# Optimization experiments

Hardware: AMD Instinct MI355X
Metric: run time of the kernel (lower is better)

The kernel has to match this reference:

```python
import jax, jax.numpy as jnp
import numpy as np

H1, W1GRID, K_SIZE, B = 28, 28, 5, 512
K2 = K_SIZE * K_SIZE  # 25 kernel weight matrices
_BITS = np.array([[0, 0], [0, 1], [1, 0], [1, 1]])  # 2^dim basis combos


def _grid_edges(h, w):
    """8-neighborhood grid graph; returns (src, dst, pseudo in [0,1]^2)."""
    ys, xs = np.meshgrid(np.arange(h), np.arange(w), indexing='ij')
    node = (ys * w + xs).reshape(-1)
    ys, xs = ys.reshape(-1), xs.reshape(-1)
    srcs, dsts, pses = [], [], []
    for dy in (-1, 0, 1):
        for dx in (-1, 0, 1):
            if dy == 0 and dx == 0:
                continue
            ny, nx = ys + dy, xs + dx
            ok = (ny >= 0) & (ny < h) & (nx >= 0) & (nx < w)
            srcs.append((ny * w + nx)[ok])   # neighbor j
            dsts.append(node[ok])            # center i
            p = np.array([[(dx + 1) / 2.0, (dy + 1) / 2.0]], dtype=np.float32)
            pses.append(np.repeat(p, ok.sum(), axis=0))
    return (np.concatenate(srcs), np.concatenate(dsts), np.concatenate(pses))


def _batched_graph(h, w, batch):
    s, d, p = _grid_edges(h, w)
    n = h * w
    off = (np.arange(batch, dtype=np.int64) * n)[:, None]
    src = (s[None, :] + off).reshape(-1)
    dst = (d[None, :] + off).reshape(-1)
    pse = np.tile(p, (batch, 1))
    return np.stack([src, dst]), pse


def setup_inputs() -> dict:
    key = jax.random.key(0)
    ks = jax.random.split(key, 8)
    e1, p1 = _batched_graph(28, 28, B)
    e2, p2 = _batched_graph(14, 14, B)
    return {
        'x': jax.random.uniform(ks[0], (B * 784, 1), jnp.float32),
        'pseudo1': jnp.asarray(p1), 'pseudo2': jnp.asarray(p2),
        'W1': jax.random.normal(ks[1], (K2, 1, 32), jnp.float32) * 0.2,
        'root1': jax.random.normal(ks[2], (1, 32), jnp.float32) * 0.2,
        'b1': jnp.zeros((32,), jnp.float32),
        'W2': jax.random.normal(ks[3], (K2, 32, 64), jnp.float32) * 0.05,
        'root2': jax.random.normal(ks[4], (32, 64), jnp.float32) * 0.05,
        'b2': jnp.zeros((64,), jnp.float32),
        'fc1_w': jax.random.normal(ks[5], (3136, 512), jnp.float32) * 0.02,
        'fc1_b': jnp.zeros((512,), jnp.float32),
        'fc2_w': jax.random.normal(ks[6], (512, 10), jnp.float32) * 0.05,
        'fc2_b': jnp.zeros((10,), jnp.float32),
        'edge_index1': jnp.asarray(e1, jnp.int64 if jax.config.jax_enable_x64 else jnp.int32),
        'edge_index2': jnp.asarray(e2, jnp.int64 if jax.config.jax_enable_x64 else jnp.int32),
    }


def _spline_basis(pseudo, k):
    # open B-spline, degree 1: each dim contributes 2 knots with linear weights
    frac = pseudo * (k - 1)                                   # [E,2]
    lo = jnp.clip(jnp.floor(frac), 0, k - 2)
    f = frac - lo                                             # [E,2]
    w = jnp.stack([1.0 - f, f], axis=-1)                      # [E,2,2]
    idx = jnp.stack([lo, lo + 1], axis=-1).astype(jnp.int32)  # [E,2,2]
    basis = w[:, 0, _BITS[:, 0]] * w[:, 1, _BITS[:, 1]]       # [E,4]
    widx = idx[:, 0, _BITS[:, 0]] + idx[:, 1, _BITS[:, 1]] * k  # [E,4]
    return basis, widx


def _spline_conv(x, edge_index, pseudo, W, root, bias, n_nodes, k):
    src, dst = edge_index[0], edge_index[1]
    x_j = x[src]                                              # [E,Cin] gather
    basis, widx = _spline_basis(pseudo, k)                    # [E,4]
    kk = k * k
    flat = (dst[:, None] * kk + widx).reshape(-1)             # [E*4]
    contrib = (basis[:, :, None] * x_j[:, None, :]).reshape(-1, x.shape[1])
    S = jnp.zeros((n_nodes * kk, x.shape[1]), x.dtype).at[flat].add(contrib)
    S = S.reshape(n_nodes, kk, x.shape[1])                    # per-node per-kernel sums
    deg = jnp.zeros((n_nodes,), x.dtype).at[dst].add(1.0)
    out = jnp.einsum('nki,kio->no', S, W) / jnp.maximum(deg, 1.0)[:, None]
    return out + x @ root + bias


def _pool2x2(x, b, hw, c):
    return x.reshape(b, hw // 2, 2, hw // 2, 2, c).max(axis=(2, 4))


def reference(x, pseudo1, pseudo2, W1, root1, b1, W2, root2, b2,
              fc1_w, fc1_b, fc2_w, fc2_b, edge_index1, edge_index2):
    n1 = x.shape[0]
    b = n1 // 784
    h = jax.nn.elu(_spline_conv(x, edge_index1, pseudo1, W1, root1, b1, n1, K_SIZE))
    h = _pool2x2(h, b, 28, 32).reshape(-1, 32)                # [B*196,32]
    h = jax.nn.elu(_spline_conv(h, edge_index2, pseudo2, W2, root2, b2, b * 196, K_SIZE))
    h = _pool2x2(h, b, 14, 64).reshape(-1, 7 * 7 * 64)        # [B,3136]
    h = jax.nn.elu(h @ fc1_w + fc1_b)
    # dropout is identity in eval mode
    h = jax.nn.elu(h @ fc2_w + fc2_b)
    return jax.nn.log_softmax(h, axis=-1)
```

## Files before the change

### kernel.cpp

```cpp
#include <hip/hip_runtime.h>
#include <math.h>

#define BATCH 512

__device__ __forceinline__ float elu1(float v) {
    return v > 0.f ? v : expm1f(v);
}

__global__ __launch_bounds__(256) void k12_conv12(
    const float* __restrict__ x, const float* __restrict__ W1,
    const float* __restrict__ root1, const float* __restrict__ b1,
    const float* __restrict__ W2, const float* __restrict__ root2,
    const float* __restrict__ b2, float* __restrict__ p2) {
    __shared__ float xs1[900];
    __shared__ float w1s[320];
    __shared__ float xs2[9216];
    __shared__ float wb[2304];
    const int b = blockIdx.x;
    const int t = threadIdx.x;

    static const int widx_t[8] = {0, 2, 4, 10, 14, 20, 22, 24};
    static const int ddy[8] = {-1,-1,-1, 0, 0, 1, 1, 1};
    static const int ddx[8] = {-1, 0, 1,-1, 1,-1, 0, 1};

    for (int l = t; l < 900; l += 256) xs1[l] = 0.f;
    {
        int d = t >> 5, c = t & 31;
        int e = d + (d >= 4 ? 1 : 0);
        int dy = e / 3 - 1, dx = e % 3 - 1;
        int widx = 2 * (dx + 1) + 10 * (dy + 1);
        w1s[t] = W1[widx * 32 + c];
        if (t < 32) { w1s[256 + t] = root1[t]; w1s[288 + t] = b1[t]; }
    }
    {
        const float4* s4 = (const float4*)W2;
        float4 v0 = s4[t], v1 = s4[t + 256];
        *(float4*)(wb + (t >> 4) * 72 + (t & 15) * 4) = v0;
        *(float4*)(wb + ((t + 256) >> 4) * 72 + (t & 15) * 4) = v1;
    }
    {
        float4 z = make_float4(0.f, 0.f, 0.f, 0.f);
        float4* x4 = (float4*)xs2;
        for (int l = t; l < 540; l += 256) {
            int nd = l / 9, s = l - nd * 9;
            int y, xx;
            if (nd < 16)      { y = 0;       xx = nd; }
            else if (nd < 32) { y = 15;      xx = nd - 16; }
            else if (nd < 46) { y = nd - 31; xx = 0; }
            else              { y = nd - 45; xx = 15; }
            x4[(y * 16 + xx) * 9 + s] = z;
        }
    }
    __syncthreads();
    {
        const float* xb = x + (size_t)b * 784;
        for (int l = t; l < 784; l += 256) {
            int y = l / 28, xx = l % 28;
            xs1[(y + 1) * 30 + xx + 1] = xb[l];
        }
    }
    __syncthreads();

    if (t < 196) {
        int py = t / 14, px = t % 14;
        int xbse[4];
        float xc[4], inv1[4];
        #pragma unroll
        for (int p = 0; p < 4; ++p) {
            int sy = p >> 1, sx = p & 1;
            int y = 2 * py + sy, xx = 2 * px + sx;
            xbse[p] = (y + 1) * 30 + xx + 1;
            xc[p] = xs1[xbse[p]];
            int nvy = 3 - (y == 0) - (y == 27);
            int nvx = 3 - (xx == 0) - (xx == 27);
            inv1[p] = 1.f / (float)(nvy * nvx - 1);
        }
        const float4* w4 = (const float4*)w1s;
        const int npw = (py + 1) * 16 + px + 1;
        const int szw = (py + 1) & 7;
        float* outp = xs2 + npw * 36;

        #pragma unroll
        for (int h = 0; h < 2; ++h) {
            float4 acc[4][4];
            #pragma unroll
            for (int p = 0; p < 4; ++p)
                #pragma unroll
                for (int q = 0; q < 4; ++q) acc[p][q] = make_float4(0.f, 0.f, 0.f, 0.f);
            #pragma unroll
            for (int d = 0; d < 8; ++d) {
                int e = d + (d >= 4 ? 1 : 0);
                int od = (e / 3 - 1) * 30 + (e % 3 - 1);
                float4 w0 = w4[d * 8 + h * 4 + 0];
                float4 w1 = w4[d * 8 + h * 4 + 1];
                float4 w2 = w4[d * 8 + h * 4 + 2];
                float4 w3 = w4[d * 8 + h * 4 + 3];
                #pragma unroll
                for (int p = 0; p < 4; ++p) {
                    float xv = xs1[xbse[p] + od];
                    acc[p][0].x += xv * w0.x; acc[p][0].y += xv * w0.y; acc[p][0].z += xv * w0.z; acc[p][0].w += xv * w0.w;
                    acc[p][1].x += xv * w1.x; acc[p][1].y += xv * w1.y; acc[p][1].z += xv * w1.z; acc[p][1].w += xv * w1.w;
                    acc[p][2].x += xv * w2.x; acc[p][2].y += xv * w2.y; acc[p][2].z += xv * w2.z; acc[p][2].w += xv * w2.w;
                    acc[p][3].x += xv * w3.x; acc[p][3].y += xv * w3.y; acc[p][3].z += xv * w3.z; acc[p][3].w += xv * w3.w;
                }
            }
            #pragma unroll
            for (int q = 0; q < 4; ++q) {
                float4 rt = w4[64 + h * 4 + q];
                float4 bs = w4[72 + h * 4 + q];
                float4 m = make_float4(-1e30f, -1e30f, -1e30f, -1e30f);
                #pragma unroll
                for (int p = 0; p < 4; ++p) {
                    float4 v;
                    v.x = elu1(acc[p][q].x * inv1[p] + xc[p] * rt.x + bs.x);
                    v.y = elu1(acc[p][q].y * inv1[p] + xc[p] * rt.y + bs.y);
                    v.z = elu1(acc[p][q].z * inv1[p] + xc[p] * rt.z + bs.z);
                    v.w = elu1(acc[p][q].w * inv1[p] + xc[p] * rt.w + bs.w);
                    m.x = fmaxf(m.x, v.x); m.y = fmaxf(m.y, v.y);
                    m.z = fmaxf(m.z, v.z); m.w = fmaxf(m.w, v.w);
                }
                int B = h * 4 + q;
                *(float4*)(outp + 4 * (B ^ szw)) = m;
            }
        }
    }
    __syncthreads();

    int tile = t >> 3; if (tile > 27) tile = 27;
    const int cg = t & 7;
    const int py2 = tile >> 2, q2 = tile & 3;
    int npb[8]; float invd[8];
    #pragma unroll
    for (int p = 0; p < 8; ++p) {
        int r = p >> 2, c = p & 3;
        int gy = 2 * py2 + r, gx = 4 * q2 + c;
        npb[p] = (gy + 1) * 16 + gx + 1;
        int gxc = gx > 13 ? 13 : gx;
        int nvy = 3 - (gy == 0) - (gy == 13);
        int nvx = 3 - (gxc == 0) - (gxc == 13);
        invd[p] = 1.f / (float)(nvy * nvx - 1);
    }

    float4 acc[8][2];
    #pragma unroll
    for (int p = 0; p < 8; ++p) { acc[p][0] = make_float4(0,0,0,0); acc[p][1] = make_float4(0,0,0,0); }

    for (int d = 0; d < 9; ++d) {
        float4 pf0, pf1;
        if (d < 8) {
            const float* nsrc = (d + 1 == 8) ? root2 : (W2 + (size_t)widx_t[d + 1] * 2048);
            pf0 = ((const float4*)nsrc)[t];
            pf1 = ((const float4*)nsrc)[t + 256];
        }
        if (d == 8) {
            #pragma unroll
            for (int p = 0; p < 8; ++p) {
                acc[p][0].x *= invd[p]; acc[p][0].y *= invd[p]; acc[p][0].z *= invd[p]; acc[p][0].w *= invd[p];
                acc[p][1].x *= invd[p]; acc[p][1].y *= invd[p]; acc[p][1].z *= invd[p]; acc[p][1].w *= invd[p];
            }
        }
        int dnode = (d < 8) ? (ddy[d] * 16 + ddx[d]) : 0;
        int ax[8], sz[8];
        #pragma unroll
        for (int p = 0; p < 8; ++p) {
            int np = npb[p] + dnode;
            ax[p] = np * 36;
            sz[p] = (np >> 4) & 7;
        }
        #pragma unroll 2
        for (int i4 = 0; i4 < 8; ++i4) {
            float xa[8][4];
            #pragma unroll
            for (int p = 0; p < 8; ++p) {
                float4 v = *(const float4*)(xs2 + ax[p] + 4 * (i4 ^ sz[p]));
                xa[p][0] = v.x; xa[p][1] = v.y; xa[p][2] = v.z; xa[p][3] = v.w;
            }
            #pragma unroll
            for (int ii = 0; ii < 4; ++ii) {
                const float* wr = wb + (i4 * 4 + ii) * 72 + cg * 8;
                float4 w0 = *(const float4*)wr;
                float4 w1 = *(const float4*)(wr + 4);
                #pragma unroll
                for (int p = 0; p < 8; ++p) {
                    float xv = xa[p][ii];
                    acc[p][0].x += xv * w0.x; acc[p][0].y += xv * w0.y;
                    acc[p][0].z += xv * w0.z; acc[p][0].w += xv * w0.w;
                    acc[p][1].x += xv * w1.x; acc[p][1].y += xv * w1.y;
                    acc[p][1].z += xv * w1.z; acc[p][1].w += xv * w1.w;
                }
            }
        }
        if (d < 8) {
            __syncthreads();
            *(float4*)(wb + (t >> 4) * 72 + (t & 15) * 4) = pf0;
            *(float4*)(wb + ((t + 256) >> 4) * 72 + (t & 15) * 4) = pf1;
            __syncthreads();
        }
    }

    if (t < 224) {
        float4 bs0 = *(const float4*)(b2 + cg * 8);
        float4 bs1 = *(const float4*)(b2 + cg * 8 + 4);
        float* outb = p2 + (size_t)b * 3136;
        #pragma unroll
        for (int cc = 0; cc < 2; ++cc) {
            int cellcol = 2 * q2 + cc;
            if (cellcol > 6) continue;
            float4 m0 = make_float4(-1e30f,-1e30f,-1e30f,-1e30f);
            float4 m1 = m0;
            #pragma unroll
            for (int r = 0; r < 2; ++r)
            #pragma unroll
            for (int c2 = 0; c2 < 2; ++c2) {
                int p = r * 4 + cc * 2 + c2;
                float4 v0, v1;
                v0.x = elu1(acc[p][0].x + bs0.x); v0.y = elu1(acc[p][0].y + bs0.y);
                v0.z = elu1(acc[p][0].z + bs0.z); v0.w = elu1(acc[p][0].w + bs0.w);
                v1.x = elu1(acc[p][1].x + bs1.x); v1.y = elu1(acc[p][1].y + bs1.y);
                v1.z = elu1(acc[p][1].z + bs1.z); v1.w = elu1(acc[p][1].w + bs1.w);
                m0.x = fmaxf(m0.x, v0.x); m0.y = fmaxf(m0.y, v0.y);
                m0.z = fmaxf(m0.z, v0.z); m0.w = fmaxf(m0.w, v0.w);
                m1.x = fmaxf(m1.x, v1.x); m1.y = fmaxf(m1.y, v1.y);
                m1.z = fmaxf(m1.z, v1.z); m1.w = fmaxf(m1.w, v1.w);
            }
            int cell = py2 * 7 + cellcol;
            *(float4*)(outb + cell * 64 + cg * 8)     = m0;
            *(float4*)(outb + cell * 64 + cg * 8 + 4) = m1;
        }
    }
}

__global__ __launch_bounds__(256) void k3a_fc1(
    const float* __restrict__ A, const float* __restrict__ B,
    float* __restrict__ part) {
    __shared__ float As[2][16][64];
    __shared__ float Bs[2][16][72];
    const int t = threadIdx.x;
    const int tx = t & 15, ty = t >> 4;
    const int n0 = blockIdx.x * 64, m0 = blockIdx.y * 64;
    const int k0 = blockIdx.z * 272;
    const int steps = ((blockIdx.z == 11) ? 144 : 272) >> 4;

    const int sm = t & 63, k4 = t >> 6;
    const int sk = t >> 4, sc = t & 15;
    const float* Ap = A + (size_t)(m0 + sm) * 3136 + k0 + k4 * 4;
    const float* Bp = B + (size_t)(k0 + sk) * 512 + n0 + sc * 4;

    {
        float4 av = *(const float4*)Ap;
        float4 bv = *(const float4*)Bp;
        As[0][k4 * 4 + 0][sm] = av.x; As[0][k4 * 4 + 1][sm] = av.y;
        As[0][k4 * 4 + 2][sm] = av.z; As[0][k4 * 4 + 3][sm] = av.w;
        *(float4*)&Bs[0][sk][sc * 4] = bv;
    }
    __syncthreads();

    float acc[4][4];
    #pragma unroll
    for (int r = 0; r < 4; ++r)
        #pragma unroll
        for (int c = 0; c < 4; ++c) acc[r][c] = 0.f;

    for (int s = 0; s < steps; ++s) {
        float4 a0, b0;
        if (s + 1 < steps) {
            a0 = *(const float4*)(Ap + (s + 1) * 16);
            b0 = *(const float4*)(Bp + (size_t)(s + 1) * 16 * 512);
        }
        const int cur = s & 1;
        #pragma unroll
        for (int k = 0; k < 16; ++k) {
            float4 a4 = *(const float4*)&As[cur][k][ty * 4];
            float4 b4 = *(const float4*)&Bs[cur][k][tx * 4];
            acc[0][0] += a4.x * b4.x; acc[0][1] += a4.x * b4.y; acc[0][2] += a4.x * b4.z; acc[0][3] += a4.x * b4.w;
            acc[1][0] += a4.y * b4.x; acc[1][1] += a4.y * b4.y; acc[1][2] += a4.y * b4.z; acc[1][3] += a4.y * b4.w;
            acc[2][0] += a4.z * b4.x; acc[2][1] += a4.z * b4.y; acc[2][2] += a4.z * b4.z; acc[2][3] += a4.z * b4.w;
            acc[3][0] += a4.w * b4.x; acc[3][1] += a4.w * b4.y; acc[3][2] += a4.w * b4.z; acc[3][3] += a4.w * b4.w;
        }
        if (s + 1 < steps) {
            const int nxt = cur ^ 1;
            As[nxt][k4 * 4 + 0][sm] = a0.x; As[nxt][k4 * 4 + 1][sm] = a0.y;
            As[nxt][k4 * 4 + 2][sm] = a0.z; As[nxt][k4 * 4 + 3][sm] = a0.w;
            *(float4*)&Bs[nxt][sk][sc * 4] = b0;
        }
        __syncthreads();
    }

    float* pbase = part + ((size_t)blockIdx.z * 512 + m0 + ty * 4) * 512 + n0;
    #pragma unroll
    for (int r = 0; r < 4; ++r)
        *(float4*)(pbase + (size_t)r * 512 + tx * 4) =
            make_float4(acc[r][0], acc[r][1], acc[r][2], acc[r][3]);
}

__global__ __launch_bounds__(256) void k34_reduce_fc2_lsm(
    const float* __restrict__ part, const float* __restrict__ fc1b,
    const float* __restrict__ w, const float* __restrict__ fc2b,
    float* __restrict__ out, int KZ) {
    __shared__ float red[4][10];
    const int b = blockIdx.x, t = threadIdx.x;

    float a0 = fc1b[t], a1 = fc1b[t + 256];
    for (int kz = 0; kz < KZ; ++kz) {
        const float* pr = part + ((size_t)kz * 512 + b) * 512;
        a0 += pr[t]; a1 += pr[t + 256];
    }
    a0 = elu1(a0); a1 = elu1(a1);

    float acc[10];
    #pragma unroll
    for (int o = 0; o < 10; ++o)
        acc[o] = a0 * w[t * 10 + o] + a1 * w[(t + 256) * 10 + o];
    #pragma unroll
    for (int s = 32; s; s >>= 1)
        #pragma unroll
        for (int o = 0; o < 10; ++o) acc[o] += __shfl_xor(acc[o], s, 64);
    if ((t & 63) == 0) {
        #pragma unroll
        for (int o = 0; o < 10; ++o) red[t >> 6][o] = acc[o];
    }
    __syncthreads();
    if (t == 0) {
        float v[10], m = -1e30f;
        #pragma unroll
        for (int o = 0; o < 10; ++o) {
            float s = red[0][o] + red[1][o] + red[2][o] + red[3][o] + fc2b[o];
            v[o] = elu1(s);
            m = fmaxf(m, v[o]);
        }
        float ssum = 0.f;
        #pragma unroll
        for (int o = 0; o < 10; ++o) ssum += expf(v[o] - m);
        float lse = m + logf(ssum);
        #pragma unroll
        for (int o = 0; o < 10; ++o) out[(size_t)b * 10 + o] = v[o] - lse;
    }
}

extern "C" void kernel_launch(void* const* d_in, const int* in_sizes, int n_in,
                              void* d_out, int out_size, void* d_ws, size_t ws_size,
                              hipStream_t stream) {
    const float* x     = (const float*)d_in[0];
    const float* W1    = (const float*)d_in[3];
    const float* root1 = (const float*)d_in[4];
    const float* b1v   = (const float*)d_in[5];
    const float* W2    = (const float*)d_in[6];
    const float* root2 = (const float*)d_in[7];
    const float* b2v   = (const float*)d_in[8];
    const float* fc1w  = (const float*)d_in[9];
    const float* fc1b  = (const float*)d_in[10];
    const float* fc2w  = (const float*)d_in[11];
    const float* fc2b  = (const float*)d_in[12];

    float* ws = (float*)d_ws;
    float* part = ws;
    float* p2 = ws + 3211264;

    k12_conv12<<<dim3(BATCH), 256, 0, stream>>>(x, W1, root1, b1v, W2, root2, b2v, p2);
    k3a_fc1<<<dim3(8, 8, 12), 256, 0, stream>>>(p2, fc1w, part);
    k34_reduce_fc2_lsm<<<dim3(BATCH), 256, 0, stream>>>(part, fc1b, fc2w, fc2b, (float*)d_out, 12);
}
```

Baseline: 118.4 us.

## Use planar channel-block LDS layout and packed FMA in conv2 inner loop

Replaces the padded, XOR-swizzled node-major LDS layout of the pooled conv1 output with a planar layout, where each of the 8 float4 channel blocks is a 256-node plane. This simplifies address computation in the conv2 inner loop and shrinks shared memory. The conv2 accumulators are also rewritten as 2-wide float vectors so the compiler can emit packed FMA instructions (v_pk_fma_f32). The planar layout drops the swizzle, which may change LDS bank-conflict behaviour for the per-node float4 reads.

```diff
diff --git a/kernel.cpp b/kernel.cpp
--- a/kernel.cpp
+++ b/kernel.cpp
@@ -2,6 +2,8 @@
 #include <math.h>
 
 #define BATCH 512
+
+typedef float v2f __attribute__((ext_vector_type(2)));
 
 __device__ __forceinline__ float elu1(float v) {
     return v > 0.f ? v : expm1f(v);
@@ -14,7 +16,7 @@
     const float* __restrict__ b2, float* __restrict__ p2) {
     __shared__ float xs1[900];
     __shared__ float w1s[320];
-    __shared__ float xs2[9216];
+    __shared__ float xs2[8192];
     __shared__ float wb[2304];
     const int b = blockIdx.x;
     const int t = threadIdx.x;
@@ -41,14 +43,14 @@
     {
         float4 z = make_float4(0.f, 0.f, 0.f, 0.f);
         float4* x4 = (float4*)xs2;
-        for (int l = t; l < 540; l += 256) {
-            int nd = l / 9, s = l - nd * 9;
+        for (int l = t; l < 480; l += 256) {
+            int nd = l >> 3, B = l & 7;
             int y, xx;
             if (nd < 16)      { y = 0;       xx = nd; }
             else if (nd < 32) { y = 15;      xx = nd - 16; }
             else if (nd < 46) { y = nd - 31; xx = 0; }
             else              { y = nd - 45; xx = 15; }
-            x4[(y * 16 + xx) * 9 + s] = z;
+            x4[B * 256 + y * 16 + xx] = z;
         }
     }
     __syncthreads();
@@ -77,8 +79,7 @@
         }
         const float4* w4 = (const float4*)w1s;
         const int npw = (py + 1) * 16 + px + 1;
-        const int szw = (py + 1) & 7;
-        float* outp = xs2 + npw * 36;
+        float4* out4 = (float4*)xs2;
 
         #pragma unroll
         for (int h = 0; h < 2; ++h) {
@@ -119,8 +120,7 @@
                     m.x = fmaxf(m.x, v.x); m.y = fmaxf(m.y, v.y);
                     m.z = fmaxf(m.z, v.z); m.w = fmaxf(m.w, v.w);
                 }
-                int B = h * 4 + q;
-                *(float4*)(outp + 4 * (B ^ szw)) = m;
+                out4[(h * 4 + q) * 256 + npw] = m;
             }
         }
     }
@@ -141,10 +141,13 @@
         invd[p] = 1.f / (float)(nvy * nvx - 1);
     }
 
-    float4 acc[8][2];
-    #pragma unroll
-    for (int p = 0; p < 8; ++p) { acc[p][0] = make_float4(0,0,0,0); acc[p][1] = make_float4(0,0,0,0); }
-
+    v2f acc2[8][4];
+    #pragma unroll
+    for (int p = 0; p < 8; ++p)
+        #pragma unroll
+        for (int j = 0; j < 4; ++j) acc2[p][j] = (v2f){0.f, 0.f};
+
+    const float4* xs4 = (const float4*)xs2;
     for (int d = 0; d < 9; ++d) {
         float4 pf0, pf1;
         if (d < 8) {
@@ -155,24 +158,22 @@
         if (d == 8) {
             #pragma unroll
             for (int p = 0; p < 8; ++p) {
-                acc[p][0].x *= invd[p]; acc[p][0].y *= invd[p]; acc[p][0].z *= invd[p]; acc[p][0].w *= invd[p];
-                acc[p][1].x *= invd[p]; acc[p][1].y *= invd[p]; acc[p][1].z *= invd[p]; acc[p][1].w *= invd[p];
+                v2f iv = {invd[p], invd[p]};
+                #pragma unroll
+                for (int j = 0; j < 4; ++j) acc2[p][j] *= iv;
             }
         }
         int dnode = (d < 8) ? (ddy[d] * 16 + ddx[d]) : 0;
-        int ax[8], sz[8];
-        #pragma unroll
-        for (int p = 0; p < 8; ++p) {
-            int np = npb[p] + dnode;
-            ax[p] = np * 36;
-            sz[p] = (np >> 4) & 7;
-        }
+        const float4* xp[8];
+        #pragma unroll
+        for (int p = 0; p < 8; ++p) xp[p] = xs4 + (npb[p] + dnode);
+
         #pragma unroll 2
         for (int i4 = 0; i4 < 8; ++i4) {
             float xa[8][4];
             #pragma unroll
             for (int p = 0; p < 8; ++p) {
-                float4 v = *(const float4*)(xs2 + ax[p] + 4 * (i4 ^ sz[p]));
+                float4 v = xp[p][i4 * 256];
                 xa[p][0] = v.x; xa[p][1] = v.y; xa[p][2] = v.z; xa[p][3] = v.w;
             }
             #pragma unroll
@@ -180,13 +181,14 @@
                 const float* wr = wb + (i4 * 4 + ii) * 72 + cg * 8;
                 float4 w0 = *(const float4*)wr;
                 float4 w1 = *(const float4*)(wr + 4);
+                v2f w2v[4] = {{w0.x, w0.y}, {w0.z, w0.w}, {w1.x, w1.y}, {w1.z, w1.w}};
                 #pragma unroll
                 for (int p = 0; p < 8; ++p) {
-                    float xv = xa[p][ii];
-                    acc[p][0].x += xv * w0.x; acc[p][0].y += xv * w0.y;
-                    acc[p][0].z += xv * w0.z; acc[p][0].w += xv * w0.w;
-                    acc[p][1].x += xv * w1.x; acc[p][1].y += xv * w1.y;
-                    acc[p][1].z += xv * w1.z; acc[p][1].w += xv * w1.w;
+                    v2f xv2 = {xa[p][ii], xa[p][ii]};
+                    acc2[p][0] += xv2 * w2v[0];
+                    acc2[p][1] += xv2 * w2v[1];
+                    acc2[p][2] += xv2 * w2v[2];
+                    acc2[p][3] += xv2 * w2v[3];
                 }
             }
         }
@@ -201,31 +203,29 @@
     if (t < 224) {
         float4 bs0 = *(const float4*)(b2 + cg * 8);
         float4 bs1 = *(const float4*)(b2 + cg * 8 + 4);
+        float bsv[8] = {bs0.x, bs0.y, bs0.z, bs0.w, bs1.x, bs1.y, bs1.z, bs1.w};
         float* outb = p2 + (size_t)b * 3136;
         #pragma unroll
         for (int cc = 0; cc < 2; ++cc) {
             int cellcol = 2 * q2 + cc;
             if (cellcol > 6) continue;
-            float4 m0 = make_float4(-1e30f,-1e30f,-1e30f,-1e30f);
-            float4 m1 = m0;
+            float mv[8];
+            #pragma unroll
+            for (int j = 0; j < 8; ++j) mv[j] = -1e30f;
             #pragma unroll
             for (int r = 0; r < 2; ++r)
             #pragma unroll
             for (int c2 = 0; c2 < 2; ++c2) {
                 int p = r * 4 + cc * 2 + c2;
-                float4 v0, v1;
-                v0.x = elu1(acc[p][0].x + bs0.x); v0.y = elu1(acc[p][0].y + bs0.y);
-                v0.z = elu1(acc[p][0].z + bs0.z); v0.w = elu1(acc[p][0].w + bs0.w);
-                v1.x = elu1(acc[p][1].x + bs1.x); v1.y = elu1(acc[p][1].y + bs1.y);
-                v1.z = elu1(acc[p][1].z + bs1.z); v1.w = elu1(acc[p][1].w + bs1.w);
-                m0.x = fmaxf(m0.x, v0.x); m0.y = fmaxf(m0.y, v0.y);
-                m0.z = fmaxf(m0.z, v0.z); m0.w = fmaxf(m0.w, v0.w);
-                m1.x = fmaxf(m1.x, v1.x); m1.y = fmaxf(m1.y, v1.y);
-                m1.z = fmaxf(m1.z, v1.z); m1.w = fmaxf(m1.w, v1.w);
+                #pragma unroll
+                for (int j = 0; j < 8; ++j) {
+                    float v = elu1(acc2[p][j >> 1][j & 1] + bsv[j]);
+                    mv[j] = fmaxf(mv[j], v);
+                }
             }
             int cell = py2 * 7 + cellcol;
-            *(float4*)(outb + cell * 64 + cg * 8)     = m0;
-            *(float4*)(outb + cell * 64 + cg * 8 + 4) = m1;
+            *(float4*)(outb + cell * 64 + cg * 8)     = make_float4(mv[0], mv[1], mv[2], mv[3]);
+            *(float4*)(outb + cell * 64 + cg * 8 + 4) = make_float4(mv[4], mv[5], mv[6], mv[7]);
         }
     }
 }
```

New measurement: 118.0 us, median of 2. About the same (-0.3%).
